# Kernel optimization log

Measured on AMD Instinct MI355X. Metric: run time of the kernel, lower is better.

## Reference

```python
import jax, jax.numpy as jnp
import numpy as np

ORDER = 24
N_POINTS = 524288


def setup_inputs() -> dict:
    key = jax.random.key(0)
    k1, k2 = jax.random.split(key)
    xyz = jax.random.uniform(k1, (N_POINTS, 3), dtype=jnp.float32)
    coeffs = jax.random.normal(k2, (ORDER ** 3,), dtype=jnp.float32) * 0.1
    return {"xyz": xyz, "coeffs": coeffs}


def reference(xyz, coeffs):
    # Faithful to: sum_{i,j,k} c[i,j,k] * sin(2pi i x) * sin(2pi j y) * sin(2pi k z)
    # but with per-axis sin tables computed once (O(order) transcendentals per point)
    # and the triple sum expressed as chained contractions (GEMM-like).
    order = ORDER
    C = coeffs.reshape(order, order, order)  # c[i,j,k]
    n = jnp.arange(order, dtype=xyz.dtype)   # frequencies 0..order-1 (i=0 row is all zeros)
    two_pi = jnp.asarray(2.0 * np.pi, dtype=xyz.dtype)
    S = jnp.sin(two_pi * xyz[:, :, None] * n)  # [N, 3, order]
    Sx, Sy, Sz = S[:, 0, :], S[:, 1, :], S[:, 2, :]  # each [N, order]
    A = jnp.einsum('nk,ijk->nij', Sz, C)   # [N, order, order]
    B = jnp.einsum('nj,nij->ni', Sy, A)    # [N, order]
    return jnp.einsum('ni,ni->n', Sx, B)   # [N]
```

## Files before the change

### kernel.cpp

```cpp
#include <hip/hip_runtime.h>

typedef _Float16 f16x2 __attribute__((ext_vector_type(2)));
typedef _Float16 f16x8 __attribute__((ext_vector_type(8)));
typedef __fp16   fp16v2 __attribute__((ext_vector_type(2)));
typedef float    f32x16 __attribute__((ext_vector_type(16)));
typedef unsigned int u32x4 __attribute__((ext_vector_type(4)));

#define TROWSTR 25

__device__ __forceinline__ f16x2 pk2(float lo, float hi) {
    fp16v2 p = __builtin_amdgcn_cvt_pkrtz(lo, hi);
    return __builtin_bit_cast(f16x2, p);
}
__device__ __forceinline__ unsigned int pkbits(f16x2 a, f16x2 b) {
    f16x2 r = a * b;
    return __builtin_bit_cast(unsigned int, r);
}

__global__ __launch_bounds__(256) void prep_B(const float* __restrict__ coeffs,
                                              f16x8* __restrict__ wsB)
{
    int chunk = blockIdx.x * 256 + threadIdx.x;
    int s = chunk >> 6, l = chunk & 63;
    int i = l & 31, h = l >> 5;
    f16x8 v;
    if (i < 24) {
        const float* src = coeffs + i * 576 + 16 * s + 8 * h;
#pragma unroll
        for (int e = 0; e < 8; ++e) v[e] = (_Float16)src[e];
    } else {
#pragma unroll
        for (int e = 0; e < 8; ++e) v[e] = (_Float16)0.f;
    }
    wsB[chunk] = v;
}

__global__ __launch_bounds__(256, 2) void fourier_main(
    const float* __restrict__ xyz,
    const f16x8* __restrict__ wsB,
    float* __restrict__ out)
{
    __shared__ __align__(16) float Tl[4 * 32 * TROWSTR];

    const int tid  = threadIdx.x;
    const int wave = tid >> 6;
    const int lane = tid & 63;
    const int h    = lane >> 5;
    const int mr   = lane & 31;
    const bool hb  = (h != 0);

    const int pw = (blockIdx.x * 4 + wave) * 128;

    f16x8 bt[36];
#pragma unroll
    for (int s = 1; s < 36; ++s) bt[s] = wsB[s * 64 + lane];

    float cx = xyz[3 * (pw + mr) + 0];
    float cy = xyz[3 * (pw + mr) + 1];
    float cz = xyz[3 * (pw + mr) + 2];

    float* Tw = Tl + wave * (32 * TROWSTR);

#pragma unroll 1
    for (int it = 0; it < 4; ++it) {
        const int pp0 = pw + it * 32;

        int pn = (it < 3) ? (pp0 + 32 + mr) : (pw + mr);
        float nx = xyz[3 * pn + 0];
        float ny = xyz[3 * pn + 1];
        float nz = xyz[3 * pn + 2];

        float s1y = __builtin_amdgcn_sinf(cy);
        float c1y = __builtin_amdgcn_cosf(cy);
        float c2y = 2.f * c1y;
        float syc = hb ? s1y : 0.f;
        float syp = hb ? 0.f : -s1y;

        float s1 = __builtin_amdgcn_sinf(cz);
        float c1 = __builtin_amdgcn_cosf(cz);
        float w8 = __builtin_amdgcn_fractf(8.f * cz);
        float s8 = __builtin_amdgcn_sinf(w8);
        float c8 = __builtin_amdgcn_cosf(w8);
        float s16 = 2.f * s8 * c8;
        float c16 = fmaf(2.f * c8, c8, -1.f);
        float c2z = 2.f * c1;

        f16x2 szR[3][4];
#pragma unroll
        for (int t = 0; t < 3; ++t) {
            float sk, ck;
            if (t == 0) { sk = hb ? s8  : 0.f;  ck = hb ? c8  : 1.f;  }
            if (t == 1) { sk = hb ? s16 : s8;   ck = hb ? c16 : c8;   }
            if (t == 2) { sk = hb ? 0.f : s16;  ck = hb ? 1.f : c16;  }
            float v[8];
            v[0] = sk;
            v[1] = fmaf(sk, c1, ck * s1);
#pragma unroll
            for (int e = 2; e < 8; ++e) v[e] = fmaf(c2z, v[e - 1], -v[e - 2]);
#pragma unroll
            for (int q = 0; q < 4; ++q) szR[t][q] = pk2(v[2 * q], v[2 * q + 1]);
        }

        f32x16 acc = {};

#pragma unroll
        for (int s = 1; s < 36; ++s) {
            const int t = (2 * s) % 3;
            f16x2 hy2 = pk2(syc, syc);
            u32x4 aw;
            aw[0] = pkbits(hy2, szR[t][0]);
            aw[1] = pkbits(hy2, szR[t][1]);
            aw[2] = pkbits(hy2, szR[t][2]);
            aw[3] = pkbits(hy2, szR[t][3]);
            f16x8 a = __builtin_bit_cast(f16x8, aw);
            acc = __builtin_amdgcn_mfma_f32_32x32x16_f16(a, bt[s], acc, 0, 0, 0);
            if (s < 35) {
                float t1 = fmaf(c2y, syc, -syp);
                if ((s % 3) == 2) { syp = syc; syc = t1; }
                else {
                    bool stay = ((s % 3) == 0) ? !hb : hb;
                    float np = stay ? syp : syc;
                    float nc = stay ? syc : t1;
                    syp = np; syc = nc;
                }
            }
        }

        if (mr < 24) {
#pragma unroll
            for (int r = 0; r < 16; ++r) {
                int row = (r & 3) + 8 * (r >> 2) + 4 * h;
                Tw[row * TROWSTR + mr] = acc[r];
            }
        }
        asm volatile("s_waitcnt lgkmcnt(0)" ::: "memory");

        {
            float sx1 = __builtin_amdgcn_sinf(cx);
            float cx1 = __builtin_amdgcn_cosf(cx);
            const float c2x = 2.f * cx1;
            float w6  = __builtin_amdgcn_fractf(6.f * cx);
            float s6  = __builtin_amdgcn_sinf(w6);
            float c6  = __builtin_amdgcn_cosf(w6);
            float s12 = 2.f * s6 * c6;
            float c12 = fmaf(2.f * c6, c6, -1.f);
            float s11 = s12 * cx1 - c12 * sx1;
            float sp = hb ? s11 : -sx1;
            float sc = hb ? s12 : 0.f;
            const float* Tr = Tw + mr * TROWSTR + 12 * h;
            float res = 0.f;
#pragma unroll
            for (int w = 0; w < 12; ++w) {
                res = fmaf(sc, Tr[w], res);
                float nxr = fmaf(c2x, sc, -sp);
                sp = sc; sc = nxr;
            }
            res += __shfl_xor(res, 32);
            if (lane < 32) out[pp0 + mr] = res;
        }

        cx = nx; cy = ny; cz = nz;
    }
}

extern "C" void kernel_launch(void* const* d_in, const int* in_sizes, int n_in,
                              void* d_out, int out_size, void* d_ws, size_t ws_size,
                              hipStream_t stream) {
    const float* xyz    = (const float*)d_in[0];
    const float* coeffs = (const float*)d_in[1];
    float* out = (float*)d_out;
    f16x8* wsB = (f16x8*)d_ws;

    prep_B<<<9, 256, 0, stream>>>(coeffs, wsB);

    const int n = in_sizes[0] / 3;
    const int grid = n / 512;
    fourier_main<<<grid, 256, 0, stream>>>(xyz, wsB, out);
}
```

Measured before the change: 32.36 us.

## Double points per wave, precompute sin(y) table, pin B fragments in registers

Each wave now handles 256 points over 8 iterations instead of 128 over 4, and the grid is halved. This amortizes the per-wave load of the 35 B-fragment registers over more points. The serial y-sine recurrence with per-step selects inside the MFMA loop is replaced by a precomputed 24-entry table computed before the loop, which takes selects off the MFMA issue path. An empty asm barrier keeps the B fragments resident in VGPRs. The risks are higher register pressure from the 24-float table and fewer blocks to fill the GPU.

```diff
diff --git a/kernel.cpp b/kernel.cpp
--- a/kernel.cpp
+++ b/kernel.cpp
@@ -49,11 +49,13 @@
     const int mr   = lane & 31;
     const bool hb  = (h != 0);
 
-    const int pw = (blockIdx.x * 4 + wave) * 128;
+    const int pw = (blockIdx.x * 4 + wave) * 256;
 
-    f16x8 bt[36];
+    u32x4 btw[36];
 #pragma unroll
-    for (int s = 1; s < 36; ++s) bt[s] = wsB[s * 64 + lane];
+    for (int s = 1; s < 36; ++s) btw[s] = ((const u32x4*)wsB)[s * 64 + lane];
+#pragma unroll
+    for (int s = 1; s < 36; ++s) asm volatile("" : "+v"(btw[s]));
 
     float cx = xyz[3 * (pw + mr) + 0];
     float cy = xyz[3 * (pw + mr) + 1];
@@ -62,10 +64,10 @@
     float* Tw = Tl + wave * (32 * TROWSTR);
 
 #pragma unroll 1
-    for (int it = 0; it < 4; ++it) {
+    for (int it = 0; it < 8; ++it) {
         const int pp0 = pw + it * 32;
 
-        int pn = (it < 3) ? (pp0 + 32 + mr) : (pw + mr);
+        int pn = (it < 7) ? (pp0 + 32 + mr) : (pw + mr);
         float nx = xyz[3 * pn + 0];
         float ny = xyz[3 * pn + 1];
         float nz = xyz[3 * pn + 2];
@@ -73,8 +75,10 @@
         float s1y = __builtin_amdgcn_sinf(cy);
         float c1y = __builtin_amdgcn_cosf(cy);
         float c2y = 2.f * c1y;
-        float syc = hb ? s1y : 0.f;
-        float syp = hb ? 0.f : -s1y;
+        float syv[24];
+        syv[0] = 0.f; syv[1] = s1y;
+#pragma unroll
+        for (int j = 2; j < 24; ++j) syv[j] = fmaf(c2y, syv[j - 1], -syv[j - 2]);
 
         float s1 = __builtin_amdgcn_sinf(cz);
         float c1 = __builtin_amdgcn_cosf(cz);
@@ -105,25 +109,19 @@
 
 #pragma unroll
         for (int s = 1; s < 36; ++s) {
-            const int t = (2 * s) % 3;
-            f16x2 hy2 = pk2(syc, syc);
+            const int t  = (2 * s) % 3;
+            const int j0 = (2 * s) / 3;
+            const int j1 = (2 * s + 1) / 3;
+            float hy = (j0 == j1) ? syv[j0] : (hb ? syv[j1] : syv[j0]);
+            f16x2 hy2 = pk2(hy, hy);
             u32x4 aw;
             aw[0] = pkbits(hy2, szR[t][0]);
             aw[1] = pkbits(hy2, szR[t][1]);
             aw[2] = pkbits(hy2, szR[t][2]);
             aw[3] = pkbits(hy2, szR[t][3]);
             f16x8 a = __builtin_bit_cast(f16x8, aw);
-            acc = __builtin_amdgcn_mfma_f32_32x32x16_f16(a, bt[s], acc, 0, 0, 0);
-            if (s < 35) {
-                float t1 = fmaf(c2y, syc, -syp);
-                if ((s % 3) == 2) { syp = syc; syc = t1; }
-                else {
-                    bool stay = ((s % 3) == 0) ? !hb : hb;
-                    float np = stay ? syp : syc;
-                    float nc = stay ? syc : t1;
-                    syp = np; syc = nc;
-                }
-            }
+            f16x8 b = __builtin_bit_cast(f16x8, btw[s]);
+            acc = __builtin_amdgcn_mfma_f32_32x32x16_f16(a, b, acc, 0, 0, 0);
         }
 
         if (mr < 24) {
@@ -174,6 +172,6 @@
     prep_B<<<9, 256, 0, stream>>>(coeffs, wsB);
 
     const int n = in_sizes[0] / 3;
-    const int grid = n / 512;
+    const int grid = n / 1024;
     fourier_main<<<grid, 256, 0, stream>>>(xyz, wsB, out);
 }
```

Result: faster. 31.69 us (-2.1%).
